# Kernel tuning notes

Measured on AMD Instinct MI355X. Metric: run time of the kernel, lower is better.

Reference implementation:

```python
import jax, jax.numpy as jnp
import numpy as np

SP, WD, H, HID = 8, 3, 8, 256
D = HID // H
TEMP = 0.1


def setup_inputs() -> dict:
    key = jax.random.key(0)
    ks = jax.random.split(key, 14)
    B, Lq, Lk, F = 4, 1024, 2048, SP + WD
    s = 0.05
    return {
        "q_fp": jax.random.normal(ks[0], (B, Lq, F), jnp.float32),
        "v_ret": jax.random.normal(ks[1], (B, Lk, F), jnp.float32),
        "pi_star": jax.random.uniform(ks[2], (B, Lq, Lk), jnp.float32),
        "Wq_s": jax.random.normal(ks[3], (HID, SP), jnp.float32) * s,
        "bq_s": jax.random.normal(ks[4], (HID,), jnp.float32) * s,
        "Wk_s": jax.random.normal(ks[5], (HID, SP), jnp.float32) * s,
        "bk_s": jax.random.normal(ks[6], (HID,), jnp.float32) * s,
        "Wq_w": jax.random.normal(ks[7], (HID, WD), jnp.float32) * s,
        "bq_w": jax.random.normal(ks[8], (HID,), jnp.float32) * s,
        "Wk_w": jax.random.normal(ks[9], (HID, WD), jnp.float32) * s,
        "bk_w": jax.random.normal(ks[10], (HID,), jnp.float32) * s,
        "Wv": jax.random.normal(ks[11], (HID, F), jnp.float32) * s,
        "bv": jnp.zeros((HID,), jnp.float32),
        "Wo": jax.random.normal(ks[12], (HID, HID), jnp.float32) * s,
        "bo": jnp.zeros((HID,), jnp.float32),
        "wave_blend": jnp.array(0.5, jnp.float32),
    }


def _proj(x, W, b):
    # x: [B, L, F_in] -> [B, H, L, D]
    B, L, _ = x.shape
    return (x @ W.T + b).reshape(B, L, H, D).transpose(0, 2, 1, 3)


def reference(q_fp, v_ret, pi_star, Wq_s, bq_s, Wk_s, bk_s, Wq_w, bq_w, Wk_w, bk_w, Wv, bv, Wo, bo, wave_blend):
    B, Lq, _ = q_fp.shape
    # split streams: first SP dims spatial, next WD dims wave (F == SP+WD)
    q_sp, q_wv = q_fp[..., :SP], q_fp[..., SP:SP + WD]
    k_sp, k_wv = v_ret[..., :SP], v_ret[..., SP:SP + WD]
    # structural branch: scaled dot product
    q_struct = _proj(q_sp, Wq_s, bq_s)
    k_struct = _proj(k_sp, Wk_s, bk_s)
    spatial_logits = jnp.einsum('bhqd,bhkd->bhqk', q_struct, k_struct) / np.float32(np.sqrt(D))
    # wave branch: negative squared euclidean distance via norm expansion
    q_wp = _proj(q_wv, Wq_w, bq_w)
    k_wp = _proj(k_wv, Wk_w, bk_w)
    qn = jnp.sum(q_wp * q_wp, axis=-1)[..., :, None]   # [B,H,Lq,1]
    kn = jnp.sum(k_wp * k_wp, axis=-1)[..., None, :]   # [B,H,1,Lk]
    qk = jnp.einsum('bhqd,bhkd->bhqk', q_wp, k_wp)
    wave_logits = -(qn + kn - 2.0 * qk) / np.float32(TEMP)
    alpha = jax.nn.sigmoid(wave_blend)
    transport_mask = jnp.log(jnp.clip(pi_star, 1e-9, None))[:, None]  # [B,1,Lq,Lk]
    attn = jax.nn.softmax((1.0 - alpha) * spatial_logits + alpha * wave_logits + transport_mask, axis=-1)
    values = _proj(v_ret, Wv, bv)  # [B,H,Lk,D]
    ctx = jnp.einsum('bhqk,bhkd->bhqd', attn, values)
    ctx = ctx.transpose(0, 2, 1, 3).reshape(B, Lq, HID)
    return ctx @ Wo.T + bo
```

## Files before the change

kernel.cpp:

```cpp
#include <hip/hip_runtime.h>
#include <hip/hip_bf16.h>
#include <cstdint>

#define B_    4
#define LQ    1024
#define LK    2048
#define FEAT  11
#define SP_   8
#define WD_   3
#define H_    8
#define HID_  256
#define LOG2E 1.4426950408889634f
#define SPLIT 4
#define KPS   (LK / SPLIT)
#define ITERS (KPS / 64)

typedef __attribute__((ext_vector_type(4))) float f32x4;
typedef __attribute__((ext_vector_type(8))) short bf16x8;
typedef __attribute__((ext_vector_type(4))) short s16x4;

__device__ __forceinline__ float sigmoidf_(float x) { return 1.f / (1.f + __expf(-x)); }

__device__ __forceinline__ short f2bf(float f) {
  unsigned u = __float_as_uint(f);
  u += 0x7fffu + ((u >> 16) & 1u);
  return (short)(u >> 16);
}
__device__ __forceinline__ float bf2f(short s) {
  return __uint_as_float(((unsigned)(unsigned short)s) << 16);
}

__device__ __forceinline__ void gl_lds16(const void* g, void* l) {
  __builtin_amdgcn_global_load_lds(
      (const __attribute__((address_space(1))) unsigned int*)g,
      (__attribute__((address_space(3))) unsigned int*)l, 16, 0, 0);
}

__global__ __launch_bounds__(256) void proj_q_kernel(
    const float* __restrict__ q_fp, const float* __restrict__ Wq_s,
    const float* __restrict__ bq_s, const float* __restrict__ Wq_w,
    const float* __restrict__ bq_w, const float* __restrict__ wb,
    short* __restrict__ Qh)
{
  const int blk = blockIdx.x, bh = blockIdx.y;
  const int b = bh >> 3, h = bh & 7;
  const int t = threadIdx.x;
  const int ql = t >> 2, part = t & 3;
  const int q = blk * 64 + ql;
  const float alpha = sigmoidf_(wb[0]);
  const float c1 = (1.f - alpha) * 0.17677669529663687f * LOG2E;
  const float c2 = 2.f * alpha * 10.f * LOG2E;

  const float* x = q_fp + (size_t)(b * LQ + q) * FEAT;
  float xs[FEAT];
  #pragma unroll
  for (int f = 0; f < FEAT; ++f) xs[f] = x[f];

  const size_t base = ((size_t)bh * LQ + q) * 64 + part * 8;
  s16x4 out_s[2], out_w[2];
  #pragma unroll
  for (int i = 0; i < 8; ++i) {
    const int dg = h * 32 + part * 8 + i;
    float s = bq_s[dg];
    #pragma unroll
    for (int f = 0; f < SP_; ++f) s += xs[f] * Wq_s[dg * SP_ + f];
    float w = bq_w[dg];
    #pragma unroll
    for (int f = 0; f < WD_; ++f) w += xs[SP_ + f] * Wq_w[dg * WD_ + f];
    out_s[i >> 2][i & 3] = f2bf(c1 * s);
    out_w[i >> 2][i & 3] = f2bf(c2 * w);
  }
  *(s16x4*)(Qh + base)          = out_s[0];
  *(s16x4*)(Qh + base + 4)      = out_s[1];
  *(s16x4*)(Qh + base + 32)     = out_w[0];
  *(s16x4*)(Qh + base + 36)     = out_w[1];
}

__global__ __launch_bounds__(256) void projk_pack_kernel(
    const float* __restrict__ v_ret, const float* __restrict__ Wk_s,
    const float* __restrict__ bk_s, const float* __restrict__ Wk_w,
    const float* __restrict__ bk_w, const float* __restrict__ Wv,
    const float* __restrict__ bv,   const float* __restrict__ wb,
    short* __restrict__ KV, float* __restrict__ kb)
{
  __shared__ float ldsv[64][33];
  const int blk = blockIdx.x, bh = blockIdx.y;
  const int b = bh >> 3, h = bh & 7;
  const int t = threadIdx.x;
  const int kl = t >> 2, part = t & 3;
  const int k = blk * 64 + kl;
  const float alpha = sigmoidf_(wb[0]);

  const float* x = v_ret + (size_t)(b * LK + k) * FEAT;
  float xs[FEAT];
  #pragma unroll
  for (int f = 0; f < FEAT; ++f) xs[f] = x[f];

  float s8[8], w8[8], v8[8];
  #pragma unroll
  for (int i = 0; i < 8; ++i) {
    const int d = h * 32 + part * 8 + i;
    float s = bk_s[d];
    #pragma unroll
    for (int f = 0; f < SP_; ++f) s += xs[f] * Wk_s[d * SP_ + f];
    float w = bk_w[d];
    #pragma unroll
    for (int f = 0; f < WD_; ++f) w += xs[SP_ + f] * Wk_w[d * WD_ + f];
    float v = bv[d];
    #pragma unroll
    for (int f = 0; f < FEAT; ++f) v += xs[f] * Wv[d * FEAT + f];
    s8[i] = s; w8[i] = w; v8[i] = v;
    ldsv[kl][part * 8 + i] = v;
  }

  float sq = 0.f;
  #pragma unroll
  for (int i = 0; i < 8; ++i) sq += w8[i] * w8[i];
  sq += __shfl_xor(sq, 1);
  sq += __shfl_xor(sq, 2);
  if (part == 0) kb[(size_t)bh * LK + k] = -10.f * alpha * LOG2E * sq;

  const int a  = kl >> 5;
  const int bb = (kl >> 2) & 1;
  const int p  = kl - a * 32 - bb * 4;
  const int lo = ((p >> 3) << 2) | (p & 3);
  const int t4 = a * 2 + bb;
  const size_t base = ((size_t)bh * 32 + blk) * 768;

  bf16x8 hs, hw;
  #pragma unroll
  for (int i = 0; i < 8; ++i) { hs[i] = f2bf(s8[i]); hw[i] = f2bf(w8[i]); }
  *(bf16x8*)(KV + (base + (t4 * 2 + 0) * 64 + part * 16 + lo) * 8) = hs;
  *(bf16x8*)(KV + (base + (t4 * 2 + 1) * 64 + part * 16 + lo) * 8) = hw;

  __syncthreads();

  {
    const int j = t >> 6, l = t & 63;
    const int dt = j >> 1, kw = j & 1;
    const int lo2 = l & 15, quad = l >> 4;
    const int d = dt * 16 + lo2;
    bf16x8 hv;
    #pragma unroll
    for (int i = 0; i < 8; ++i)
      hv[i] = f2bf(ldsv[kw * 32 + quad * 8 + i][d]);
    *(bf16x8*)(KV + (base + 512 + t) * 8) = hv;
  }
}

union PF { int i[4]; bf16x8 v; };

__device__ __forceinline__ void attn_step2(
    const short* __restrict__ cbuf, const bf16x8 qh[2][2],
    const float* __restrict__ pib0, const float* __restrict__ pib1,
    const float* __restrict__ kbp, const bf16x8 ones, int lane,
    float m[2], f32x4 o[2][2], f32x4 ol[2])
{
  f32x4 pi4[2][4];
  pi4[0][0] = *(const f32x4*)(pib0);
  pi4[0][1] = *(const f32x4*)(pib0 + 4);
  pi4[0][2] = *(const f32x4*)(pib0 + 32);
  pi4[0][3] = *(const f32x4*)(pib0 + 36);
  pi4[1][0] = *(const f32x4*)(pib1);
  pi4[1][1] = *(const f32x4*)(pib1 + 4);
  pi4[1][2] = *(const f32x4*)(pib1 + 32);
  pi4[1][3] = *(const f32x4*)(pib1 + 36);
  f32x4 kb4[4];
  kb4[0] = *(const f32x4*)(kbp);
  kb4[1] = *(const f32x4*)(kbp + 4);
  kb4[2] = *(const f32x4*)(kbp + 32);
  kb4[3] = *(const f32x4*)(kbp + 36);

  f32x4 st[2][4];
  #pragma unroll
  for (int t4 = 0; t4 < 4; ++t4) {
    const bf16x8 ka0 = *(const bf16x8*)(cbuf + ((t4 * 2 + 0) * 64 + lane) * 8);
    const bf16x8 ka1 = *(const bf16x8*)(cbuf + ((t4 * 2 + 1) * 64 + lane) * 8);
    #pragma unroll
    for (int tl = 0; tl < 2; ++tl) {
      f32x4 z = {0.f, 0.f, 0.f, 0.f};
      z = __builtin_amdgcn_mfma_f32_16x16x32_bf16(ka0, qh[tl][0], z, 0, 0, 0);
      z = __builtin_amdgcn_mfma_f32_16x16x32_bf16(ka1, qh[tl][1], z, 0, 0, 0);
      st[tl][t4] = z;
    }
  }

  const bf16x8 va00 = *(const bf16x8*)(cbuf + ((512 + 0 * 64) + lane) * 8);
  const bf16x8 va01 = *(const bf16x8*)(cbuf + ((512 + 1 * 64) + lane) * 8);
  const bf16x8 va10 = *(const bf16x8*)(cbuf + ((512 + 2 * 64) + lane) * 8);
  const bf16x8 va11 = *(const bf16x8*)(cbuf + ((512 + 3 * 64) + lane) * 8);

  #pragma unroll
  for (int tl = 0; tl < 2; ++tl) {
    float lg[16];
    #pragma unroll
    for (int t4 = 0; t4 < 4; ++t4) {
      #pragma unroll
      for (int r = 0; r < 4; ++r) lg[t4 * 4 + r] = st[tl][t4][r] + kb4[t4][r];
    }

    float cm = lg[0];
    #pragma unroll
    for (int j = 1; j < 16; ++j) cm = fmaxf(cm, lg[j]);
    cm = fmaxf(cm, __shfl_xor(cm, 16));
    cm = fmaxf(cm, __shfl_xor(cm, 32));
    const float mn = fmaxf(m[tl], cm);
    const float sc = __builtin_amdgcn_exp2f(m[tl] - mn);
    m[tl] = mn;

    unsigned eu[16];
    #pragma unroll
    for (int t4 = 0; t4 < 4; ++t4) {
      #pragma unroll
      for (int r = 0; r < 4; ++r)
        eu[t4 * 4 + r] = __float_as_uint(
            __builtin_amdgcn_exp2f(lg[t4 * 4 + r] - mn) * pi4[tl][t4][r]);
    }

    PF pf0, pf1;
    #pragma unroll
    for (int p = 0; p < 4; ++p) {
      pf0.i[p] = __builtin_amdgcn_perm(eu[2 * p + 1], eu[2 * p], 0x07060302u);
      pf1.i[p] = __builtin_amdgcn_perm(eu[8 + 2 * p + 1], eu[8 + 2 * p], 0x07060302u);
    }

    #pragma unroll
    for (int r = 0; r < 4; ++r) { o[tl][0][r] *= sc; o[tl][1][r] *= sc; ol[tl][r] *= sc; }

    o[tl][0] = __builtin_amdgcn_mfma_f32_16x16x32_bf16(va00, pf0.v, o[tl][0], 0, 0, 0);
    o[tl][0] = __builtin_amdgcn_mfma_f32_16x16x32_bf16(va01, pf1.v, o[tl][0], 0, 0, 0);
    o[tl][1] = __builtin_amdgcn_mfma_f32_16x16x32_bf16(va10, pf0.v, o[tl][1], 0, 0, 0);
    o[tl][1] = __builtin_amdgcn_mfma_f32_16x16x32_bf16(va11, pf1.v, o[tl][1], 0, 0, 0);
    ol[tl] = __builtin_amdgcn_mfma_f32_16x16x32_bf16(ones, pf0.v, ol[tl], 0, 0, 0);
    ol[tl] = __builtin_amdgcn_mfma_f32_16x16x32_bf16(ones, pf1.v, ol[tl], 0, 0, 0);
  }
}

__global__ __launch_bounds__(256, 4) void attn_kernel(
    const short* __restrict__ Qh, const short* __restrict__ KV,
    const float* __restrict__ kb, const float* __restrict__ pi,
    float* __restrict__ part)
{
  __shared__ short skv[2][6144];
  const int id = blockIdx.x;
  const int combo = id & 127;
  const int qblk  = id >> 7;
  const int bh = combo >> 2;
  const int sp = combo & 3;
  const int b = bh >> 3;
  const int wv = threadIdx.x >> 6;
  const int lane = threadIdx.x & 63;
  const int lo16 = lane & 15;
  const int quad = lane >> 4;
  const int qt0 = qblk * 8 + wv * 2;
  const int blk0 = sp * ITERS;

  bf16x8 qh[2][2];
  #pragma unroll
  for (int tl = 0; tl < 2; ++tl) {
    const size_t qoff = ((size_t)bh * LQ + (qt0 + tl) * 16 + lo16) * 64 + quad * 8;
    qh[tl][0] = *(const bf16x8*)(Qh + qoff);
    qh[tl][1] = *(const bf16x8*)(Qh + qoff + 32);
  }

  const float* pib0 = pi + ((size_t)(b * LQ + qt0 * 16 + lo16)) * LK
                      + sp * KPS + quad * 8;
  const float* pib1 = pib0 + (size_t)16 * LK;
  const float* kbbase = kb + (size_t)bh * LK + sp * KPS + quad * 8;

  bf16x8 ones;
  #pragma unroll
  for (int j = 0; j < 8; ++j) ones[j] = (lo16 == 0) ? (short)0x3F80 : (short)0;

  float m[2] = {-1e30f, -1e30f};
  f32x4 o[2][2] = {{{0.f,0.f,0.f,0.f},{0.f,0.f,0.f,0.f}},
                   {{0.f,0.f,0.f,0.f},{0.f,0.f,0.f,0.f}}};
  f32x4 ol[2] = {{0.f,0.f,0.f,0.f},{0.f,0.f,0.f,0.f}};

  {
    const size_t gb = ((size_t)bh * 32 + blk0) * 768;
    #pragma unroll
    for (int c = 0; c < 3; ++c)
      gl_lds16(KV + (gb + c * 256 + wv * 64 + lane) * 8,
               &skv[0][c * 2048 + wv * 512]);
  }

  for (int it = 0; it < ITERS; it += 2) {
    __syncthreads();
    {
      const size_t gb = ((size_t)bh * 32 + blk0 + it + 1) * 768;
      #pragma unroll
      for (int c = 0; c < 3; ++c)
        gl_lds16(KV + (gb + c * 256 + wv * 64 + lane) * 8,
                 &skv[1][c * 2048 + wv * 512]);
    }
    attn_step2(skv[0], qh, pib0 + it * 64, pib1 + it * 64,
               kbbase + it * 64, ones, lane, m, o, ol);

    __syncthreads();
    if (it + 2 < ITERS) {
      const size_t gb = ((size_t)bh * 32 + blk0 + it + 2) * 768;
      #pragma unroll
      for (int c = 0; c < 3; ++c)
        gl_lds16(KV + (gb + c * 256 + wv * 64 + lane) * 8,
                 &skv[0][c * 2048 + wv * 512]);
    }
    attn_step2(skv[1], qh, pib0 + (it + 1) * 64, pib1 + (it + 1) * 64,
               kbbase + (it + 1) * 64, ones, lane, m, o, ol);
  }

  #pragma unroll
  for (int tl = 0; tl < 2; ++tl) {
    const int q = (qt0 + tl) * 16 + lo16;
    float* ppart = part + ((size_t)(sp * 32 + bh) * LQ + q) * 36;
    if (quad == 0) { ppart[0] = m[tl]; ppart[1] = ol[tl][0]; }
    *(f32x4*)(ppart + 4 + quad * 4)  = o[tl][0];
    *(f32x4*)(ppart + 20 + quad * 4) = o[tl][1];
  }
}

__global__ __launch_bounds__(256) void wo_prep_kernel(
    const float* __restrict__ Wo, short* __restrict__ WoH, short* __restrict__ WoL)
{
  const int i = (blockIdx.x * 256 + threadIdx.x) * 4;
  const f32x4 v = *(const f32x4*)(Wo + i);
  s16x4 h, l;
  #pragma unroll
  for (int j = 0; j < 4; ++j) {
    h[j] = f2bf(v[j]);
    l[j] = f2bf(v[j] - bf2f(h[j]));
  }
  *(s16x4*)(WoH + i) = h;
  *(s16x4*)(WoL + i) = l;
}

__global__ __launch_bounds__(256) void out_kernel(
    const float* __restrict__ part, const short* __restrict__ WoH,
    const short* __restrict__ WoL, const float* __restrict__ bo,
    float* __restrict__ out)
{
  const int t = threadIdx.x;
  const int wv = t >> 6, lane = t & 63;
  const int lo16 = lane & 15, quad = lane >> 4;
  const int mt = blockIdx.x;
  const size_t gq = (size_t)mt * 16 + lo16;
  const int b = (int)(gq >> 10), qq = (int)(gq & (LQ - 1));

  bf16x8 Ah[8], Al[8];
  #pragma unroll
  for (int win = 0; win < 8; ++win) {
    const size_t r = (size_t)(b * H_ + win) * LQ + qq;
    const float* p[SPLIT];
    float ms[SPLIT], ls[SPLIT];
    #pragma unroll
    for (int s = 0; s < SPLIT; ++s) {
      p[s] = part + (r + (size_t)s * (B_ * H_ * LQ)) * 36;
      ms[s] = p[s][0]; ls[s] = p[s][1];
    }
    float mM = ms[0];
    #pragma unroll
    for (int s = 1; s < SPLIT; ++s) mM = fmaxf(mM, ms[s]);
    float ws[SPLIT], den = 0.f;
    #pragma unroll
    for (int s = 0; s < SPLIT; ++s) {
      ws[s] = __builtin_amdgcn_exp2f(ms[s] - mM);
      den += ws[s] * ls[s];
    }
    const float inv = 1.f / den;

    float c8[8];
    #pragma unroll
    for (int j = 0; j < 8; ++j) c8[j] = 0.f;
    #pragma unroll
    for (int s = 0; s < SPLIT; ++s) {
      const f32x4 a0 = *(const f32x4*)(p[s] + 4 + quad * 8);
      const f32x4 a1 = *(const f32x4*)(p[s] + 8 + quad * 8);
      #pragma unroll
      for (int j = 0; j < 4; ++j) {
        c8[j]     += ws[s] * a0[j];
        c8[4 + j] += ws[s] * a1[j];
      }
    }
    #pragma unroll
    for (int j = 0; j < 8; ++j) {
      const float cv = c8[j] * inv;
      const short hi = f2bf(cv);
      Ah[win][j] = hi;
      Al[win][j] = f2bf(cv - bf2f(hi));
    }
  }

  const int n0 = wv * 64;
  #pragma unroll
  for (int nt = 0; nt < 4; ++nt) {
    const int nb = n0 + nt * 16;
    const short* bh = WoH + (size_t)(nb + lo16) * HID_ + quad * 8;
    const short* bl = WoL + (size_t)(nb + lo16) * HID_ + quad * 8;
    const float bias = bo[nb + lo16];
    f32x4 acc = {bias, bias, bias, bias};
    #pragma unroll
    for (int win = 0; win < 8; ++win) {
      const bf16x8 Bh = *(const bf16x8*)(bh + win * 32);
      const bf16x8 Bl = *(const bf16x8*)(bl + win * 32);
      acc = __builtin_amdgcn_mfma_f32_16x16x32_bf16(Ah[win], Bh, acc, 0, 0, 0);
      acc = __builtin_amdgcn_mfma_f32_16x16x32_bf16(Al[win], Bh, acc, 0, 0, 0);
      acc = __builtin_amdgcn_mfma_f32_16x16x32_bf16(Ah[win], Bl, acc, 0, 0, 0);
    }
    #pragma unroll
    for (int r4 = 0; r4 < 4; ++r4)
      out[(size_t)(mt * 16 + quad * 4 + r4) * HID_ + nb + lo16] = acc[r4];
  }
}

extern "C" void kernel_launch(void* const* d_in, const int* in_sizes, int n_in,
                              void* d_out, int out_size, void* d_ws, size_t ws_size,
                              hipStream_t stream)
{
  const float* q_fp  = (const float*)d_in[0];
  const float* v_ret = (const float*)d_in[1];
  const float* pi    = (const float*)d_in[2];
  const float* Wq_s  = (const float*)d_in[3];
  const float* bq_s  = (const float*)d_in[4];
  const float* Wk_s  = (const float*)d_in[5];
  const float* bk_s  = (const float*)d_in[6];
  const float* Wq_w  = (const float*)d_in[7];
  const float* bq_w  = (const float*)d_in[8];
  const float* Wk_w  = (const float*)d_in[9];
  const float* bk_w  = (const float*)d_in[10];
  const float* Wv    = (const float*)d_in[11];
  const float* bv    = (const float*)d_in[12];
  const float* Wo    = (const float*)d_in[13];
  const float* bo    = (const float*)d_in[14];
  const float* wb    = (const float*)d_in[15];
  float* out = (float*)d_out;

  short* Qh   = (short*)d_ws;
  short* KV   = Qh + (size_t)2097152;
  float* kbuf = (float*)(KV + (size_t)6291456);
  float* part = kbuf + (size_t)65536;
  short* WoH  = (short*)(part + (size_t)4718592);
  short* WoL  = WoH + (size_t)65536;

  proj_q_kernel<<<dim3(LQ / 64, 32), 256, 0, stream>>>(
      q_fp, Wq_s, bq_s, Wq_w, bq_w, wb, Qh);
  projk_pack_kernel<<<dim3(LK / 64, 32), 256, 0, stream>>>(
      v_ret, Wk_s, bk_s, Wk_w, bk_w, Wv, bv, wb, KV, kbuf);
  attn_kernel<<<(LQ / 128) * 32 * SPLIT, 256, 0, stream>>>(Qh, KV, kbuf, pi, part);
  wo_prep_kernel<<<64, 256, 0, stream>>>(Wo, WoH, WoL);
  out_kernel<<<(B_ * LQ) / 16, 256, 0, stream>>>(part, WoH, WoL, bo, out);
}
```

Measured before the change: 183.2 us.

## Prepack pi_star into bf16 MFMA-ordered tiles and stage out_kernel combine via LDS

A new pre-pass converts pi_star from fp32 into bf16 tiles laid out in MFMA lane order. The attention kernel can then fetch pi with contiguous 16-byte loads, and at half the bytes, instead of strided fp32 loads from each of the 8 heads. The out_kernel now combines the split partials once per (row, head) across threads and shares the bf16 hi/lo operands through LDS, so each lane no longer recomputes the combine for all heads. The trade-off is an extra full pass over the 32 MB pi tensor plus a 16 MB bf16 copy, and pi is rounded to bf16.

```diff
diff --git a/kernel.cpp b/kernel.cpp
--- a/kernel.cpp
+++ b/kernel.cpp
@@ -70,10 +70,10 @@
     out_s[i >> 2][i & 3] = f2bf(c1 * s);
     out_w[i >> 2][i & 3] = f2bf(c2 * w);
   }
-  *(s16x4*)(Qh + base)          = out_s[0];
-  *(s16x4*)(Qh + base + 4)      = out_s[1];
-  *(s16x4*)(Qh + base + 32)     = out_w[0];
-  *(s16x4*)(Qh + base + 36)     = out_w[1];
+  *(s16x4*)(Qh + base)      = out_s[0];
+  *(s16x4*)(Qh + base + 4)  = out_s[1];
+  *(s16x4*)(Qh + base + 32) = out_w[0];
+  *(s16x4*)(Qh + base + 36) = out_w[1];
 }
 
 __global__ __launch_bounds__(256) void projk_pack_kernel(
@@ -96,7 +96,7 @@
   #pragma unroll
   for (int f = 0; f < FEAT; ++f) xs[f] = x[f];
 
-  float s8[8], w8[8], v8[8];
+  float s8[8], w8[8];
   #pragma unroll
   for (int i = 0; i < 8; ++i) {
     const int d = h * 32 + part * 8 + i;
@@ -109,7 +109,7 @@
     float v = bv[d];
     #pragma unroll
     for (int f = 0; f < FEAT; ++f) v += xs[f] * Wv[d * FEAT + f];
-    s8[i] = s; w8[i] = w; v8[i] = v;
+    s8[i] = s; w8[i] = w;
     ldsv[kl][part * 8 + i] = v;
   }
 
@@ -148,23 +148,40 @@
   }
 }
 
+__global__ __launch_bounds__(256) void pi_prepack_kernel(
+    const float* __restrict__ pi, short* __restrict__ piB)
+{
+  const int Gid = blockIdx.x * 256 + threadIdx.x;
+  const int g    = Gid & 127;
+  const int kblk = (Gid >> 7) & 31;
+  const int qt   = (Gid >> 12) & 63;
+  const int b    = Gid >> 18;
+  const int pair = g >> 6;
+  const int quad = (g >> 4) & 3, lo = g & 15;
+  const int q = qt * 16 + lo;
+  const int k = kblk * 64 + pair * 32 + quad * 8;
+  const float* src = pi + ((size_t)(b * LQ + q) * LK + k);
+  const f32x4 v0 = *(const f32x4*)(src);
+  const f32x4 v1 = *(const f32x4*)(src + 4);
+  bf16x8 hv;
+  #pragma unroll
+  for (int j = 0; j < 4; ++j) { hv[j] = f2bf(v0[j]); hv[4 + j] = f2bf(v1[j]); }
+  *(bf16x8*)(piB + (size_t)Gid * 8) = hv;
+}
+
 union PF { int i[4]; bf16x8 v; };
 
 __device__ __forceinline__ void attn_step2(
     const short* __restrict__ cbuf, const bf16x8 qh[2][2],
-    const float* __restrict__ pib0, const float* __restrict__ pib1,
+    const short* __restrict__ pit0, const short* __restrict__ pit1,
     const float* __restrict__ kbp, const bf16x8 ones, int lane,
     float m[2], f32x4 o[2][2], f32x4 ol[2])
 {
-  f32x4 pi4[2][4];
-  pi4[0][0] = *(const f32x4*)(pib0);
-  pi4[0][1] = *(const f32x4*)(pib0 + 4);
-  pi4[0][2] = *(const f32x4*)(pib0 + 32);
-  pi4[0][3] = *(const f32x4*)(pib0 + 36);
-  pi4[1][0] = *(const f32x4*)(pib1);
-  pi4[1][1] = *(const f32x4*)(pib1 + 4);
-  pi4[1][2] = *(const f32x4*)(pib1 + 32);
-  pi4[1][3] = *(const f32x4*)(pib1 + 36);
+  bf16x8 pg[2][2];
+  pg[0][0] = *(const bf16x8*)(pit0);
+  pg[0][1] = *(const bf16x8*)(pit0 + 512);
+  pg[1][0] = *(const bf16x8*)(pit1);
+  pg[1][1] = *(const bf16x8*)(pit1 + 512);
   f32x4 kb4[4];
   kb4[0] = *(const f32x4*)(kbp);
   kb4[1] = *(const f32x4*)(kbp + 4);
@@ -210,11 +227,9 @@
 
     unsigned eu[16];
     #pragma unroll
-    for (int t4 = 0; t4 < 4; ++t4) {
-      #pragma unroll
-      for (int r = 0; r < 4; ++r)
-        eu[t4 * 4 + r] = __float_as_uint(
-            __builtin_amdgcn_exp2f(lg[t4 * 4 + r] - mn) * pi4[tl][t4][r]);
+    for (int j = 0; j < 16; ++j) {
+      const float pif = bf2f(pg[tl][j >> 3][j & 7]);
+      eu[j] = __float_as_uint(__builtin_amdgcn_exp2f(lg[j] - mn) * pif);
     }
 
     PF pf0, pf1;
@@ -238,7 +253,7 @@
 
 __global__ __launch_bounds__(256, 4) void attn_kernel(
     const short* __restrict__ Qh, const short* __restrict__ KV,
-    const float* __restrict__ kb, const float* __restrict__ pi,
+    const float* __restrict__ kb, const short* __restrict__ piB,
     float* __restrict__ part)
 {
   __shared__ short skv[2][6144];
@@ -263,9 +278,8 @@
     qh[tl][1] = *(const bf16x8*)(Qh + qoff + 32);
   }
 
-  const float* pib0 = pi + ((size_t)(b * LQ + qt0 * 16 + lo16)) * LK
-                      + sp * KPS + quad * 8;
-  const float* pib1 = pib0 + (size_t)16 * LK;
+  const short* pit0 = piB + ((((size_t)(b * 64 + qt0) * 32) + blk0) * 128 + lane) * 8;
+  const short* pit1 = piB + ((((size_t)(b * 64 + qt0 + 1) * 32) + blk0) * 128 + lane) * 8;
   const float* kbbase = kb + (size_t)bh * LK + sp * KPS + quad * 8;
 
   bf16x8 ones;
@@ -294,7 +308,7 @@
         gl_lds16(KV + (gb + c * 256 + wv * 64 + lane) * 8,
                  &skv[1][c * 2048 + wv * 512]);
     }
-    attn_step2(skv[0], qh, pib0 + it * 64, pib1 + it * 64,
+    attn_step2(skv[0], qh, pit0 + it * 1024, pit1 + it * 1024,
                kbbase + it * 64, ones, lane, m, o, ol);
 
     __syncthreads();
@@ -305,7 +319,7 @@
         gl_lds16(KV + (gb + c * 256 + wv * 64 + lane) * 8,
                  &skv[0][c * 2048 + wv * 512]);
     }
-    attn_step2(skv[1], qh, pib0 + (it + 1) * 64, pib1 + (it + 1) * 64,
+    attn_step2(skv[1], qh, pit0 + (it + 1) * 1024, pit1 + (it + 1) * 1024,
                kbbase + (it + 1) * 64, ones, lane, m, o, ol);
   }
 
@@ -339,17 +353,18 @@
     const short* __restrict__ WoL, const float* __restrict__ bo,
     float* __restrict__ out)
 {
+  __shared__ short lA[2][8 * 64 * 8];
   const int t = threadIdx.x;
-  const int wv = t >> 6, lane = t & 63;
-  const int lo16 = lane & 15, quad = lane >> 4;
   const int mt = blockIdx.x;
-  const size_t gq = (size_t)mt * 16 + lo16;
-  const int b = (int)(gq >> 10), qq = (int)(gq & (LQ - 1));
-
-  bf16x8 Ah[8], Al[8];
-  #pragma unroll
-  for (int win = 0; win < 8; ++win) {
+
+  {
+    const int win = t >> 5;
+    const int row = (t >> 1) & 15;
+    const int qp  = t & 1;
+    const size_t gq = (size_t)mt * 16 + row;
+    const int b = (int)(gq >> 10), qq = (int)(gq & (LQ - 1));
     const size_t r = (size_t)(b * H_ + win) * LQ + qq;
+
     const float* p[SPLIT];
     float ms[SPLIT], ls[SPLIT];
     #pragma unroll
@@ -368,26 +383,45 @@
     }
     const float inv = 1.f / den;
 
-    float c8[8];
-    #pragma unroll
-    for (int j = 0; j < 8; ++j) c8[j] = 0.f;
-    #pragma unroll
-    for (int s = 0; s < SPLIT; ++s) {
-      const f32x4 a0 = *(const f32x4*)(p[s] + 4 + quad * 8);
-      const f32x4 a1 = *(const f32x4*)(p[s] + 8 + quad * 8);
-      #pragma unroll
-      for (int j = 0; j < 4; ++j) {
-        c8[j]     += ws[s] * a0[j];
-        c8[4 + j] += ws[s] * a1[j];
+    #pragma unroll
+    for (int q2 = 0; q2 < 2; ++q2) {
+      const int quad = qp * 2 + q2;
+      float c8[8];
+      #pragma unroll
+      for (int j = 0; j < 8; ++j) c8[j] = 0.f;
+      #pragma unroll
+      for (int s = 0; s < SPLIT; ++s) {
+        const f32x4 a0 = *(const f32x4*)(p[s] + 4 + quad * 8);
+        const f32x4 a1 = *(const f32x4*)(p[s] + 8 + quad * 8);
+        #pragma unroll
+        for (int j = 0; j < 4; ++j) {
+          c8[j]     += ws[s] * a0[j];
+          c8[4 + j] += ws[s] * a1[j];
+        }
       }
-    }
-    #pragma unroll
-    for (int j = 0; j < 8; ++j) {
-      const float cv = c8[j] * inv;
-      const short hi = f2bf(cv);
-      Ah[win][j] = hi;
-      Al[win][j] = f2bf(cv - bf2f(hi));
-    }
+      bf16x8 ah, al;
+      #pragma unroll
+      for (int j = 0; j < 8; ++j) {
+        const float cv = c8[j] * inv;
+        const short hi = f2bf(cv);
+        ah[j] = hi;
+        al[j] = f2bf(cv - bf2f(hi));
+      }
+      const int gidx = (win * 64 + quad * 16 + row) * 8;
+      *(bf16x8*)(&lA[0][gidx]) = ah;
+      *(bf16x8*)(&lA[1][gidx]) = al;
+    }
+  }
+  __syncthreads();
+
+  const int wv = t >> 6, lane = t & 63;
+  const int lo16 = lane & 15, quad = lane >> 4;
+
+  bf16x8 Ah[8], Al[8];
+  #pragma unroll
+  for (int win = 0; win < 8; ++win) {
+    Ah[win] = *(const bf16x8*)(&lA[0][(win * 64 + lane) * 8]);
+    Al[win] = *(const bf16x8*)(&lA[1][(win * 64 + lane) * 8]);
   }
 
   const int n0 = wv * 64;
@@ -437,7 +471,8 @@
   short* Qh   = (short*)d_ws;
   short* KV   = Qh + (size_t)2097152;
   float* kbuf = (float*)(KV + (size_t)6291456);
-  float* part = kbuf + (size_t)65536;
+  short* piB  = (short*)(kbuf + (size_t)65536);
+  float* part = (float*)(piB + (size_t)8388608);
   short* WoH  = (short*)(part + (size_t)4718592);
   short* WoL  = WoH + (size_t)65536;
 
@@ -445,7 +480,8 @@
       q_fp, Wq_s, bq_s, Wq_w, bq_w, wb, Qh);
   projk_pack_kernel<<<dim3(LK / 64, 32), 256, 0, stream>>>(
       v_ret, Wk_s, bk_s, Wk_w, bk_w, Wv, bv, wb, KV, kbuf);
-  attn_kernel<<<(LQ / 128) * 32 * SPLIT, 256, 0, stream>>>(Qh, KV, kbuf, pi, part);
+  pi_prepack_kernel<<<4096, 256, 0, stream>>>(pi, piB);
+  attn_kernel<<<(LQ / 128) * 32 * SPLIT, 256, 0, stream>>>(Qh, KV, kbuf, piB, part);
   wo_prep_kernel<<<64, 256, 0, stream>>>(Wo, WoH, WoL);
   out_kernel<<<(B_ * LQ) / 16, 256, 0, stream>>>(part, WoH, WoL, bo, out);
 }
```

Measured after the change: 177.2 us. 1.03x faster.
